# Kernel tuning notes

Hardware: AMD Instinct MI355X
Metric: run time of the kernel (lower is better)

## Reference

```python
import jax, jax.numpy as jnp
import numpy as np
from jax import lax

N_ROIS = 1024
ROI_H, ROI_W = 112, 224   # height divisible by 7; band = 16 rows
BANDS = 7
POOL_H, POOL_W = 8, 16    # adaptive max pool target
CONF_THRES = 0.25
PROV, ALPHA, AD = 38, 25, 35
FLAT = 16 * (POOL_H // 2) * (POOL_W // 2)  # 512 after conv+2x2 maxpool


def setup_inputs() -> dict:
    key = jax.random.key(0)
    ks = jax.random.split(key, 16)
    x = jax.random.normal(ks[0], (1, 3, 1024, 1024), dtype=jnp.float32)
    x1 = jax.random.randint(ks[1], (N_ROIS,), 0, 1024 - ROI_W)
    y1 = jax.random.randint(ks[2], (N_ROIS,), 0, 1024 - ROI_H)
    rois = jnp.stack([x1, y1, x1 + ROI_W, y1 + ROI_H], axis=-1).astype(jnp.int32)
    detection_targets = jax.random.randint(ks[3], (N_ROIS,), 0, PROV).astype(jnp.int32)
    classification_targets = jax.random.randint(ks[4], (N_ROIS, 8), 0, ALPHA).astype(jnp.int32)
    conv_w = jax.random.normal(ks[5], (16, 3, 3, 3), dtype=jnp.float32) * 0.1
    conv_b = jnp.zeros((16,), dtype=jnp.float32)
    w1 = jax.random.normal(ks[6], (8, FLAT, 128), dtype=jnp.float32) * 0.05
    b1 = jnp.zeros((8, 128), dtype=jnp.float32)
    w2_prov = jax.random.normal(ks[7], (128, PROV), dtype=jnp.float32) * 0.05
    b2_prov = jnp.zeros((PROV,), dtype=jnp.float32)
    w2_alpha = jax.random.normal(ks[8], (128, ALPHA), dtype=jnp.float32) * 0.05
    b2_alpha = jnp.zeros((ALPHA,), dtype=jnp.float32)
    w2_ad = jax.random.normal(ks[9], (6, 128, AD), dtype=jnp.float32) * 0.05
    b2_ad = jnp.zeros((6, AD), dtype=jnp.float32)
    return dict(x=x, rois=rois, detection_targets=detection_targets,
                classification_targets=classification_targets,
                conv_w=conv_w, conv_b=conv_b, w1=w1, b1=b1,
                w2_prov=w2_prov, b2_prov=b2_prov,
                w2_alpha=w2_alpha, b2_alpha=b2_alpha,
                w2_ad=w2_ad, b2_ad=b2_ad)


def _ce(logits, tgt):
    # per-row cross entropy; matches nn.CrossEntropyLoss on batch of 1 (mean==single)
    lp = jax.nn.log_softmax(logits, axis=-1)
    return -jnp.take_along_axis(lp, tgt[:, None], axis=1)[:, 0]


def _forward(x, rois, detection_targets, classification_targets,
             conv_w, conv_b, w1, b1, w2_prov, b2_prov,
             w2_alpha, b2_alpha, w2_ad, b2_ad):
    n = rois.shape[0]
    m = n * BANDS

    def extract(roi):
        return lax.dynamic_slice(x[0], (0, roi[1], roi[0]), (3, ROI_H, ROI_W))

    crops = jax.vmap(extract)(rois)                       # (N,3,112,224)
    band_h = ROI_H // BANDS                                # 16
    sub = crops.reshape(n, 3, BANDS, band_h, ROI_W)
    sub = sub.transpose(0, 2, 1, 3, 4).reshape(m, 3, band_h, ROI_W)  # (M,3,16,224)
    # adaptive max pool (16,224) -> (8,16): exact 2x14 windows
    pooled = sub.reshape(m, 3, POOL_H, band_h // POOL_H, POOL_W, ROI_W // POOL_W).max(axis=(3, 5))

    feat = lax.conv_general_dilated(pooled, conv_w, (1, 1), 'SAME',
                                    dimension_numbers=('NCHW', 'OIHW', 'NCHW'))
    feat = jax.nn.relu(feat + conv_b[None, :, None, None])  # (M,16,8,16)
    feat = feat.reshape(m, 16, POOL_H // 2, 2, POOL_W // 2, 2).max(axis=(3, 5))  # (M,16,4,8)
    flat = feat.reshape(m, FLAT)                             # (M,512)

    h = jax.nn.relu(jnp.einsum('md,kdh->kmh', flat, w1) + b1[:, None, :])  # (8,M,128)
    out_prov = h[0] @ w2_prov + b2_prov                      # (M,38)
    out_alpha = h[1] @ w2_alpha + b2_alpha                   # (M,25)
    out_ad = jnp.einsum('kmh,khc->kmc', h[2:], w2_ad) + b2_ad[:, None, :]  # (6,M,35)

    det_t = jnp.repeat(detection_targets, BANDS)             # (M,)
    det_loss = _ce(out_prov, det_t)
    mask = det_loss < CONF_THRES

    cls_t = jnp.repeat(classification_targets, BANDS, axis=0)  # (M,8)
    cls_loss = _ce(out_prov, cls_t[:, 0]) + _ce(out_alpha, cls_t[:, 1])
    cls_loss = cls_loss + jax.vmap(_ce)(out_ad, cls_t[:, 2:].T).sum(axis=0)
    total = jnp.sum(jnp.where(mask, cls_loss, 0.0))
    return out_prov, out_alpha, out_ad, mask, total


def reference(x, rois, detection_targets, classification_targets,
              conv_w, conv_b, w1, b1, w2_prov, b2_prov,
              w2_alpha, b2_alpha, w2_ad, b2_ad):
    return _forward(x, rois, detection_targets, classification_targets,
                    conv_w, conv_b, w1, b1, w2_prov, b2_prov,
                    w2_alpha, b2_alpha, w2_ad, b2_ad)
```

## Files before the change

### kernel.cpp

```cpp
#include <hip/hip_runtime.h>

#define NROIS 1024
#define BANDS 7
#define M_TOT (NROIS*BANDS)
#define ROI_W 224
#define BAND_H 16
#define FLATD 512
#define HD 1024
#define PROV 38
#define ALPHA 25
#define ADC 35
#define NAD 6

#define OFF_A     (M_TOT*PROV)
#define OFF_AD    (OFF_A + M_TOT*ALPHA)
#define OFF_MASK  (OFF_AD + NAD*M_TOT*ADC)
#define OFF_TOTAL (OFF_MASK + M_TOT)

typedef __attribute__((ext_vector_type(4))) float f32x4;
typedef __attribute__((ext_vector_type(2))) float f32x2;
typedef __attribute__((ext_vector_type(8))) short bf16x8;

static __device__ __forceinline__ unsigned short f2bf(float f){
    union { float f; unsigned int u; } v; v.f = f;
    unsigned int u = v.u;
    unsigned int r = (u + 0x7fffu + ((u >> 16) & 1u)) >> 16;
    return (unsigned short)r;
}

#define GL16(gp, lp) __builtin_amdgcn_global_load_lds( \
    (const __attribute__((address_space(1))) unsigned int*)(gp), \
    (__attribute__((address_space(3))) unsigned int*)(lp), 16, 0, 0)

#define P2ROW(c,row) (((size_t)((c)*1023 + (row)))*1022)

__global__ __launch_bounds__(256) void k_pre_cvt(
    const float* __restrict__ x, const float* __restrict__ w1,
    const float* __restrict__ w2p, const float* __restrict__ b2p,
    const float* __restrict__ w2a, const float* __restrict__ b2a,
    const float* __restrict__ w2ad, const float* __restrict__ b2ad,
    float* __restrict__ P, unsigned short* __restrict__ Bt,
    unsigned short* __restrict__ B2, float* __restrict__ bias2)
{
    __shared__ float v[1024];
    int blk = blockIdx.x;
    int t = threadIdx.x;
    if (blk < 3069){
        int c = blk / 1023, r = blk - c*1023;
        const float* row0 = x + ((size_t)c*1024 + r)*1024;
        const float* row1 = row0 + 1024;
        #pragma unroll
        for (int i=0;i<4;i++){
            int j = t + i*256;
            v[j] = fmaxf(row0[j], row1[j]);
        }
        __syncthreads();
        float* Pr = P + P2ROW(c, r);
        #pragma unroll
        for (int i=0;i<4;i++){
            int o = t + i*256;
            if (o < 1022){
                int s = o / 73, q = o - s*73;
                int j = 14*q + s;
                if (j < 1011){
                    float mv = v[j];
                    #pragma unroll
                    for (int d=1;d<14;d++) mv = fmaxf(mv, v[j+d]);
                    Pr[o] = mv;
                }
            }
        }
    } else {
        int i = (blk - 3069)*256 + t;
        if (i < 524288){
            int k = i >> 10, n = i & 1023;
            float val = w1[((size_t)(n>>7)*512 + k)*128 + (n&127)];
            Bt[(size_t)n*512 + k] = f2bf(val);
        } else {
            int j = i - 524288;
            int h = j / 6144;
            int rem = j - h*6144;
            int n = rem >> 7, k = rem & 127;
            float val = 0.f;
            if (h == 0){ if (n < 38) val = w2p[k*38 + n]; }
            else if (h == 1){ if (n < 25) val = w2a[k*25 + n]; }
            else { if (n < 35) val = w2ad[(size_t)(h-2)*128*35 + k*35 + n]; }
            B2[j] = f2bf(val);
            if (j < 8*48){
                int hh = j / 48, nn = j - hh*48;
                float bv = 0.f;
                if (hh == 0){ if (nn < 38) bv = b2p[nn]; }
                else if (hh == 1){ if (nn < 25) bv = b2a[nn]; }
                else { if (nn < 35) bv = b2ad[(hh-2)*35 + nn]; }
                bias2[j] = bv;
            }
        }
    }
}

__global__ __launch_bounds__(256) void k_extract(
    const float* __restrict__ P, const int* __restrict__ rois,
    const float* __restrict__ conv_w, const float* __restrict__ conv_b,
    unsigned short* __restrict__ flat)
{
    __shared__ float pl[3][10][20];
    __shared__ float cw[432];
    __shared__ float cb[16];

    int r = blockIdx.x;
    int t = threadIdx.x;
    int xx = rois[r*4+0];
    int y1 = rois[r*4+1];
    int sx = xx % 14, qx = xx / 14;
    int o2 = t >> 5, p = (t >> 3) & 3, q = t & 7;

    for (int i=t;i<432;i+=256) cw[i]=conv_w[i];
    if (t<16) cb[t]=conv_b[t];
    for (int i=t;i<3*10*20;i+=256) ((float*)pl)[i]=0.f;
    __syncthreads();

    float w[2][27];
    #pragma unroll
    for (int oi=0;oi<2;oi++){
        int o = o2 + oi*8;
        #pragma unroll
        for (int k=0;k<27;k++) w[oi][k] = cw[o*27 + k];
    }
    float bias0 = cb[o2], bias1 = cb[o2+8];

    for (int b=0; b<BANDS; b++){
        int yy = y1 + b*BAND_H;
        for (int idx=t; idx<384; idx+=256){
            int c = idx>>7; int rem = idx&127; int ph = rem>>4; int pw = rem&15;
            pl[c][ph+1][pw+1] = P[P2ROW(c, yy + 2*ph) + (size_t)sx*73 + qx + pw];
        }
        __syncthreads();

        float s0[4] = {bias0,bias0,bias0,bias0};
        float s1[4] = {bias1,bias1,bias1,bias1};
        #pragma unroll
        for (int c=0;c<3;c++){
            float pt[4][4];
            #pragma unroll
            for (int di=0; di<4; di++){
                f32x2 a = *(const f32x2*)&pl[c][2*p+di][2*q];
                f32x2 bb = *(const f32x2*)&pl[c][2*p+di][2*q+2];
                pt[di][0]=a.x; pt[di][1]=a.y; pt[di][2]=bb.x; pt[di][3]=bb.y;
            }
            #pragma unroll
            for (int kh=0;kh<3;kh++)
              #pragma unroll
              for (int kw=0;kw<3;kw++){
                float w0 = w[0][c*9+kh*3+kw];
                float w1v = w[1][c*9+kh*3+kw];
                #pragma unroll
                for (int pos=0;pos<4;pos++){
                    float pv = pt[kh + (pos>>1)][kw + (pos&1)];
                    s0[pos] += pv*w0;
                    s1[pos] += pv*w1v;
                }
              }
        }
        float mx0 = fmaxf(fmaxf(fmaxf(s0[0],s0[1]), fmaxf(s0[2],s0[3])), 0.f);
        float mx1 = fmaxf(fmaxf(fmaxf(s1[0],s1[1]), fmaxf(s1[2],s1[3])), 0.f);
        size_t base = ((size_t)r*BANDS + b)*512;
        flat[base + t]       = f2bf(mx0);
        flat[base + t + 256] = f2bf(mx1);
        __syncthreads();
    }
}

__global__ __launch_bounds__(256) void k_fc1_heads(
    const unsigned short* __restrict__ A, const unsigned short* __restrict__ Bt,
    const float* __restrict__ b1, const unsigned short* __restrict__ B2,
    const float* __restrict__ bias2, float* __restrict__ out,
    float* __restrict__ lse_ws)
{
    __shared__ short smem[16896];
    short* As = smem;
    short* Bs = smem + 8192;
    short* Hl = smem;

    int bm = blockIdx.x, h = blockIdx.y;
    int m0 = bm*128;
    int t = threadIdx.x;
    int wid = t >> 6, lane = t & 63;
    int wr = wid >> 1, wc = wid & 1;
    int l15 = lane & 15, l4 = lane >> 4;

    if (bm == 0 && h == 0 && t == 0) out[OFF_TOTAL] = 0.f;

    const unsigned short* gA = A  + ((size_t)(m0    + wid*16 + (lane>>2)))*FLATD + (lane&3)*8;
    const unsigned short* gB = Bt + ((size_t)(h*128 + wid*16 + (lane>>2)))*FLATD + (lane&3)*8;

    f32x4 acc[4][4];
    #pragma unroll
    for (int i=0;i<4;i++)
      #pragma unroll
      for (int j=0;j<4;j++) acc[i][j] = (f32x4){0.f,0.f,0.f,0.f};

    GL16(gA,            As + wid*512);
    GL16(gA + 64*FLATD, As + 2048 + wid*512);
    GL16(gB,            Bs + wid*512);
    GL16(gB + 64*FLATD, Bs + 2048 + wid*512);
    __syncthreads();

    #pragma unroll
    for (int ks=0; ks<16; ks++){
        int cur = ks & 1;
        if (ks < 15){
            int k1 = (ks+1)*32;
            int nb = (cur^1)*4096;
            GL16(gA + k1,            As + nb + wid*512);
            GL16(gA + 64*FLATD + k1, As + nb + 2048 + wid*512);
            GL16(gB + k1,            Bs + nb + wid*512);
            GL16(gB + 64*FLATD + k1, Bs + nb + 2048 + wid*512);
        }
        bf16x8 af[4], bfv[4];
        #pragma unroll
        for (int mf=0;mf<4;mf++) af[mf]  = *(const bf16x8*)&As[cur*4096 + (wr*64 + mf*16 + l15)*32 + l4*8];
        #pragma unroll
        for (int nf=0;nf<4;nf++) bfv[nf] = *(const bf16x8*)&Bs[cur*4096 + (wc*64 + nf*16 + l15)*32 + l4*8];
        #pragma unroll
        for (int mf=0;mf<4;mf++)
          #pragma unroll
          for (int nf=0;nf<4;nf++)
            acc[mf][nf] = __builtin_amdgcn_mfma_f32_16x16x32_bf16(af[mf], bfv[nf], acc[mf][nf], 0, 0, 0);
        __syncthreads();
    }

    #pragma unroll
    for (int nf=0;nf<4;nf++){
        int col = wc*64 + nf*16 + l15;
        float bias = b1[h*128 + col];
        #pragma unroll
        for (int mf=0;mf<4;mf++){
            #pragma unroll
            for (int reg=0;reg<4;reg++){
                int row = wr*64 + mf*16 + l4*4 + reg;
                Hl[row*132 + col] = (short)f2bf(fmaxf(acc[mf][nf][reg] + bias, 0.f));
            }
        }
    }
    __syncthreads();

    f32x4 acc2[2][3];
    #pragma unroll
    for (int i=0;i<2;i++)
      #pragma unroll
      for (int j=0;j<3;j++) acc2[i][j] = (f32x4){0.f,0.f,0.f,0.f};

    const unsigned short* Bh = B2 + (size_t)h*6144;
    #pragma unroll
    for (int ks=0; ks<4; ks++){
        bf16x8 ha[2], hb[3];
        #pragma unroll
        for (int m2=0;m2<2;m2++)
            ha[m2] = *(const bf16x8*)&Hl[(wid*32 + m2*16 + l15)*132 + ks*32 + l4*8];
        #pragma unroll
        for (int nf=0;nf<3;nf++)
            hb[nf] = *(const bf16x8*)(Bh + (nf*16 + l15)*128 + ks*32 + l4*8);
        #pragma unroll
        for (int m2=0;m2<2;m2++)
          #pragma unroll
          for (int nf=0;nf<3;nf++)
            acc2[m2][nf] = __builtin_amdgcn_mfma_f32_16x16x32_bf16(ha[m2], hb[nf], acc2[m2][nf], 0, 0, 0);
    }

    int Nh = (h==0) ? 38 : ((h==1) ? 25 : 35);
    #pragma unroll
    for (int nf=0;nf<3;nf++){
        int col = nf*16 + l15;
        float bv = bias2[h*48 + col];
        #pragma unroll
        for (int m2=0;m2<2;m2++){
            #pragma unroll
            for (int reg=0;reg<4;reg++){
                acc2[m2][nf][reg] += bv;
                if (col < Nh){
                    int m = m0 + wid*32 + m2*16 + l4*4 + reg;
                    size_t a;
                    if (h == 0)      a = (size_t)m*38 + col;
                    else if (h == 1) a = OFF_A + (size_t)m*25 + col;
                    else             a = OFF_AD + ((size_t)(h-2)*M_TOT + m)*35 + col;
                    out[a] = acc2[m2][nf][reg];
                }
            }
        }
    }

    #pragma unroll
    for (int m2=0;m2<2;m2++){
        #pragma unroll
        for (int reg=0;reg<4;reg++){
            float mx = -1e30f;
            #pragma unroll
            for (int nf=0;nf<3;nf++){
                int col = nf*16 + l15;
                if (col < Nh) mx = fmaxf(mx, acc2[m2][nf][reg]);
            }
            #pragma unroll
            for (int d=1; d<16; d<<=1) mx = fmaxf(mx, __shfl_xor(mx, d));
            float s = 0.f;
            #pragma unroll
            for (int nf=0;nf<3;nf++){
                int col = nf*16 + l15;
                if (col < Nh) s += __expf(acc2[m2][nf][reg] - mx);
            }
            #pragma unroll
            for (int d=1; d<16; d<<=1) s += __shfl_xor(s, d);
            if (l15 == 0){
                int m = m0 + wid*32 + m2*16 + l4*4 + reg;
                lse_ws[(size_t)m*8 + h] = mx + __logf(s);
            }
        }
    }
}

__global__ __launch_bounds__(256) void k_loss(
    const float* __restrict__ lse_ws, const int* __restrict__ det_t,
    const int* __restrict__ cls_t, float* __restrict__ out)
{
    int m = blockIdx.x*256 + threadIdx.x;
    if (m >= M_TOT) return;
    int r = m / 7;
    const float* L = lse_ws + (size_t)m*8;
    float det_loss = L[0] - out[(size_t)m*38 + det_t[r]];
    bool mk = det_loss < 0.25f;
    out[OFF_MASK + m] = mk ? 1.f : 0.f;
    if (mk){
        const int* ct = cls_t + r*8;
        float c = (L[0] - out[(size_t)m*38 + ct[0]]) + (L[1] - out[OFF_A + (size_t)m*25 + ct[1]]);
        #pragma unroll
        for (int j=0;j<6;j++)
            c += L[2+j] - out[OFF_AD + ((size_t)j*M_TOT + m)*35 + ct[2+j]];
        atomicAdd(out + OFF_TOTAL, c);
    }
}

extern "C" void kernel_launch(void* const* d_in, const int* in_sizes, int n_in,
                              void* d_out, int out_size, void* d_ws, size_t ws_size,
                              hipStream_t stream) {
    const float* x      = (const float*)d_in[0];
    const int*   rois   = (const int*)d_in[1];
    const int*   det    = (const int*)d_in[2];
    const int*   cls    = (const int*)d_in[3];
    const float* conv_w = (const float*)d_in[4];
    const float* conv_b = (const float*)d_in[5];
    const float* w1     = (const float*)d_in[6];
    const float* b1     = (const float*)d_in[7];
    const float* w2p    = (const float*)d_in[8];
    const float* b2p    = (const float*)d_in[9];
    const float* w2a    = (const float*)d_in[10];
    const float* b2a    = (const float*)d_in[11];
    const float* w2ad   = (const float*)d_in[12];
    const float* b2ad   = (const float*)d_in[13];
    float* out = (float*)d_out;

    char* w = (char*)d_ws;
    unsigned short* flatbf = (unsigned short*)w;
    unsigned short* BtW    = (unsigned short*)(w + 7340032);
    unsigned short* B2     = (unsigned short*)(w + 8388608);
    float*  bias2          = (float*)(w + 8486912);
    float*  lse            = (float*)(w + 8488448);
    float*  P              = (float*)(w + 8717824);

    k_pre_cvt<<<3069 + 2240, 256, 0, stream>>>(x, w1, w2p, b2p, w2a, b2a, w2ad, b2ad,
                                               P, BtW, B2, bias2);
    k_extract<<<NROIS, 256, 0, stream>>>(P, rois, conv_w, conv_b, flatbf);
    k_fc1_heads<<<dim3(56, 8), 256, 0, stream>>>(flatbf, BtW, b1, B2, bias2, out, lse);
    k_loss<<<28, 256, 0, stream>>>(lse, det, cls, out);
}
```

Before: 134.0 us.

## Triple-buffer fc1 GEMM with swizzled LDS, batch ROI band loads, share pooling windows

The fc1 GEMM now keeps three stages in flight instead of two, using explicit vmcnt waits and raw barriers, and XOR-swizzles its LDS layout to reduce bank conflicts. In k_extract all seven band tiles of a ROI are loaded into shared memory once up front, which removes the per-band barriers. The pooling step in k_pre_cvt computes two adjacent window outputs per thread and reuses their shared 13-element max. k_loss is launched with smaller blocks so more workgroups are spread across the device. These changes raise LDS use and rely on hand-set waitcnt values that have to match the number of issued loads.

Result: slower. 138.1 us (+3.0%).

```diff
diff --git a/kernel.cpp b/kernel.cpp
--- a/kernel.cpp
+++ b/kernel.cpp
@@ -57,16 +57,19 @@
         __syncthreads();
         float* Pr = P + P2ROW(c, r);
         #pragma unroll
-        for (int i=0;i<4;i++){
-            int o = t + i*256;
-            if (o < 1022){
-                int s = o / 73, q = o - s*73;
+        for (int ii=0; ii<2; ii++){
+            int i = t + ii*256;
+            if (i < 511){
+                int s2 = i / 73, q = i - s2*73;
+                int s = 2*s2;
                 int j = 14*q + s;
                 if (j < 1011){
-                    float mv = v[j];
+                    float core = v[j+1];
                     #pragma unroll
-                    for (int d=1;d<14;d++) mv = fmaxf(mv, v[j+d]);
-                    Pr[o] = mv;
+                    for (int d=2; d<14; d++) core = fmaxf(core, v[j+d]);
+                    Pr[s*73 + q] = fmaxf(core, v[j]);
+                    if (j+1 < 1011)
+                        Pr[(s+1)*73 + q] = fmaxf(core, v[j+14]);
                 }
             }
         }
@@ -103,7 +106,7 @@
     const float* __restrict__ conv_w, const float* __restrict__ conv_b,
     unsigned short* __restrict__ flat)
 {
-    __shared__ float pl[3][10][20];
+    __shared__ float pl[3][BANDS][10][20];
     __shared__ float cw[432];
     __shared__ float cb[16];
 
@@ -116,26 +119,27 @@
 
     for (int i=t;i<432;i+=256) cw[i]=conv_w[i];
     if (t<16) cb[t]=conv_b[t];
-    for (int i=t;i<3*10*20;i+=256) ((float*)pl)[i]=0.f;
+    for (int i=t;i<3*BANDS*10*20;i+=256) ((float*)pl)[i]=0.f;
     __syncthreads();
 
+    for (int idx=t; idx<3*BANDS*8*16; idx+=256){
+        int pw = idx & 15;
+        int rem = idx >> 4;
+        int ph = rem & 7;
+        int bb = (rem >> 3) % BANDS;
+        int c  = rem / (8*BANDS);
+        pl[c][bb][ph+1][pw+1] = P[P2ROW(c, y1 + bb*BAND_H + 2*ph) + (size_t)sx*73 + qx + pw];
+    }
+    __syncthreads();
+
     float w[2][27];
     #pragma unroll
-    for (int oi=0;oi<2;oi++){
-        int o = o2 + oi*8;
-        #pragma unroll
-        for (int k=0;k<27;k++) w[oi][k] = cw[o*27 + k];
-    }
+    for (int oi=0;oi<2;oi++)
+      #pragma unroll
+      for (int k=0;k<27;k++) w[oi][k] = cw[(o2 + oi*8)*27 + k];
     float bias0 = cb[o2], bias1 = cb[o2+8];
 
     for (int b=0; b<BANDS; b++){
-        int yy = y1 + b*BAND_H;
-        for (int idx=t; idx<384; idx+=256){
-            int c = idx>>7; int rem = idx&127; int ph = rem>>4; int pw = rem&15;
-            pl[c][ph+1][pw+1] = P[P2ROW(c, yy + 2*ph) + (size_t)sx*73 + qx + pw];
-        }
-        __syncthreads();
-
         float s0[4] = {bias0,bias0,bias0,bias0};
         float s1[4] = {bias1,bias1,bias1,bias1};
         #pragma unroll
@@ -143,9 +147,9 @@
             float pt[4][4];
             #pragma unroll
             for (int di=0; di<4; di++){
-                f32x2 a = *(const f32x2*)&pl[c][2*p+di][2*q];
-                f32x2 bb = *(const f32x2*)&pl[c][2*p+di][2*q+2];
-                pt[di][0]=a.x; pt[di][1]=a.y; pt[di][2]=bb.x; pt[di][3]=bb.y;
+                f32x2 a  = *(const f32x2*)&pl[c][b][2*p+di][2*q];
+                f32x2 bb2 = *(const f32x2*)&pl[c][b][2*p+di][2*q+2];
+                pt[di][0]=a.x; pt[di][1]=a.y; pt[di][2]=bb2.x; pt[di][3]=bb2.y;
             }
             #pragma unroll
             for (int kh=0;kh<3;kh++)
@@ -166,7 +170,6 @@
         size_t base = ((size_t)r*BANDS + b)*512;
         flat[base + t]       = f2bf(mx0);
         flat[base + t + 256] = f2bf(mx1);
-        __syncthreads();
     }
 }
 
@@ -176,9 +179,9 @@
     const float* __restrict__ bias2, float* __restrict__ out,
     float* __restrict__ lse_ws)
 {
-    __shared__ short smem[16896];
+    __shared__ short smem[24576];
     short* As = smem;
-    short* Bs = smem + 8192;
+    short* Bs = smem + 12288;
     short* Hl = smem;
 
     int bm = blockIdx.x, h = blockIdx.y;
@@ -190,8 +193,10 @@
 
     if (bm == 0 && h == 0 && t == 0) out[OFF_TOTAL] = 0.f;
 
-    const unsigned short* gA = A  + ((size_t)(m0    + wid*16 + (lane>>2)))*FLATD + (lane&3)*8;
-    const unsigned short* gB = Bt + ((size_t)(h*128 + wid*16 + (lane>>2)))*FLATD + (lane&3)*8;
+    int lrow = lane >> 2;
+    int lch  = (lane & 3) ^ (lrow & 3);
+    const unsigned short* gA = A  + ((size_t)(m0    + wid*16 + lrow))*FLATD + lch*8;
+    const unsigned short* gB = Bt + ((size_t)(h*128 + wid*16 + lrow))*FLATD + lch*8;
 
     f32x4 acc[4][4];
     #pragma unroll
@@ -199,35 +204,46 @@
       #pragma unroll
       for (int j=0;j<4;j++) acc[i][j] = (f32x4){0.f,0.f,0.f,0.f};
 
-    GL16(gA,            As + wid*512);
-    GL16(gA + 64*FLATD, As + 2048 + wid*512);
-    GL16(gB,            Bs + wid*512);
-    GL16(gB + 64*FLATD, Bs + 2048 + wid*512);
-    __syncthreads();
+#define STAGE(ks, buf) do { int _k0 = (ks)*32; \
+    GL16(gA + _k0,            As + (buf)*4096 + wid*512); \
+    GL16(gA + 64*FLATD + _k0, As + (buf)*4096 + 2048 + wid*512); \
+    GL16(gB + _k0,            Bs + (buf)*4096 + wid*512); \
+    GL16(gB + 64*FLATD + _k0, Bs + (buf)*4096 + 2048 + wid*512); } while(0)
+
+    STAGE(0, 0);
+    STAGE(1, 1);
 
     #pragma unroll
     for (int ks=0; ks<16; ks++){
-        int cur = ks & 1;
-        if (ks < 15){
-            int k1 = (ks+1)*32;
-            int nb = (cur^1)*4096;
-            GL16(gA + k1,            As + nb + wid*512);
-            GL16(gA + 64*FLATD + k1, As + nb + 2048 + wid*512);
-            GL16(gB + k1,            Bs + nb + wid*512);
-            GL16(gB + 64*FLATD + k1, Bs + nb + 2048 + wid*512);
-        }
+        if (ks < 14) STAGE(ks+2, (ks+2)%3);
+        if (ks < 14)       asm volatile("s_waitcnt vmcnt(8)" ::: "memory");
+        else if (ks == 14) asm volatile("s_waitcnt vmcnt(4)" ::: "memory");
+        else               asm volatile("s_waitcnt vmcnt(0)" ::: "memory");
+        __builtin_amdgcn_s_barrier();
+        __builtin_amdgcn_sched_barrier(0);
+        int cur = ks % 3;
         bf16x8 af[4], bfv[4];
         #pragma unroll
-        for (int mf=0;mf<4;mf++) af[mf]  = *(const bf16x8*)&As[cur*4096 + (wr*64 + mf*16 + l15)*32 + l4*8];
-        #pragma unroll
-        for (int nf=0;nf<4;nf++) bfv[nf] = *(const bf16x8*)&Bs[cur*4096 + (wc*64 + nf*16 + l15)*32 + l4*8];
+        for (int mf=0;mf<4;mf++){
+            int row = wr*64 + mf*16 + l15;
+            af[mf]  = *(const bf16x8*)&As[cur*4096 + row*32 + ((l4 ^ (l15&3))*8)];
+        }
+        #pragma unroll
+        for (int nf=0;nf<4;nf++){
+            int row = wc*64 + nf*16 + l15;
+            bfv[nf] = *(const bf16x8*)&Bs[cur*4096 + row*32 + ((l4 ^ (l15&3))*8)];
+        }
         #pragma unroll
         for (int mf=0;mf<4;mf++)
           #pragma unroll
           for (int nf=0;nf<4;nf++)
             acc[mf][nf] = __builtin_amdgcn_mfma_f32_16x16x32_bf16(af[mf], bfv[nf], acc[mf][nf], 0, 0, 0);
-        __syncthreads();
-    }
+        __builtin_amdgcn_sched_barrier(0);
+        __builtin_amdgcn_s_barrier();
+    }
+#undef STAGE
+
+    __syncthreads();
 
     #pragma unroll
     for (int nf=0;nf<4;nf++){
@@ -317,11 +333,11 @@
     }
 }
 
-__global__ __launch_bounds__(256) void k_loss(
+__global__ __launch_bounds__(64) void k_loss(
     const float* __restrict__ lse_ws, const int* __restrict__ det_t,
     const int* __restrict__ cls_t, float* __restrict__ out)
 {
-    int m = blockIdx.x*256 + threadIdx.x;
+    int m = blockIdx.x*64 + threadIdx.x;
     if (m >= M_TOT) return;
     int r = m / 7;
     const float* L = lse_ws + (size_t)m*8;
@@ -369,5 +385,5 @@
                                                P, BtW, B2, bias2);
     k_extract<<<NROIS, 256, 0, stream>>>(P, rois, conv_w, conv_b, flatbf);
     k_fc1_heads<<<dim3(56, 8), 256, 0, stream>>>(flatbf, BtW, b1, B2, bias2, out, lse);
-    k_loss<<<28, 256, 0, stream>>>(lse, det, cls, out);
-}
+    k_loss<<<112, 64, 0, stream>>>(lse, det, cls, out);
+}
```

## Tile w1 transpose through LDS, share pooling windows, preload all bands

Applied to the files above, without the earlier changes.

The w1 bf16 transpose now goes through a padded 64x64 LDS tile, so both global reads and writes are coalesced and far fewer blocks are launched. The horizontal 14-wide max pooling computes two adjacent outputs per thread that share 13 elements, roughly halving the LDS max work. k_extract loads all seven bands of pooled input into shared memory in one pass and drops the per-band barriers. k_loss uses smaller blocks to spread across more CUs. The costs are more shared memory per extract block and more complex index math.

Measured after the change: 137.0 us. 1.02x slower.

```diff
diff --git a/kernel.cpp b/kernel.cpp
--- a/kernel.cpp
+++ b/kernel.cpp
@@ -42,10 +42,11 @@
     float* __restrict__ P, unsigned short* __restrict__ Bt,
     unsigned short* __restrict__ B2, float* __restrict__ bias2)
 {
-    __shared__ float v[1024];
+    __shared__ float sm[64*65];
     int blk = blockIdx.x;
     int t = threadIdx.x;
     if (blk < 3069){
+        float* v = sm;
         int c = blk / 1023, r = blk - c*1023;
         const float* row0 = x + ((size_t)c*1024 + r)*1024;
         const float* row1 = row0 + 1024;
@@ -57,43 +58,59 @@
         __syncthreads();
         float* Pr = P + P2ROW(c, r);
         #pragma unroll
-        for (int i=0;i<4;i++){
-            int o = t + i*256;
-            if (o < 1022){
-                int s = o / 73, q = o - s*73;
+        for (int ii=0; ii<2; ii++){
+            int i = t + ii*256;
+            if (i < 511){
+                int s2 = i / 73, q = i - s2*73;
+                int s = 2*s2;
                 int j = 14*q + s;
                 if (j < 1011){
-                    float mv = v[j];
+                    float core = v[j+1];
                     #pragma unroll
-                    for (int d=1;d<14;d++) mv = fmaxf(mv, v[j+d]);
-                    Pr[o] = mv;
+                    for (int d=2; d<14; d++) core = fmaxf(core, v[j+d]);
+                    Pr[s*73 + q] = fmaxf(core, v[j]);
+                    if (j+1 < 1011)
+                        Pr[(s+1)*73 + q] = fmaxf(core, v[j+14]);
                 }
             }
         }
+    } else if (blk < 3197){
+        int tt = blk - 3069;
+        int h  = tt >> 4;
+        int rem = tt & 15;
+        int k0 = (rem >> 1) * 64;
+        int n0 = (rem & 1) * 64;
+        const float* W = w1 + (size_t)h*65536;
+        #pragma unroll
+        for (int e=0;e<16;e++){
+            int idx = e*256 + t;
+            int kk = idx >> 6, nn = idx & 63;
+            sm[kk*65 + nn] = W[(size_t)(k0+kk)*128 + n0 + nn];
+        }
+        __syncthreads();
+        #pragma unroll
+        for (int e=0;e<16;e++){
+            int idx = e*256 + t;
+            int nn = idx >> 6, kk = idx & 63;
+            Bt[(size_t)(h*128 + n0 + nn)*512 + k0 + kk] = f2bf(sm[kk*65 + nn]);
+        }
     } else {
-        int i = (blk - 3069)*256 + t;
-        if (i < 524288){
-            int k = i >> 10, n = i & 1023;
-            float val = w1[((size_t)(n>>7)*512 + k)*128 + (n&127)];
-            Bt[(size_t)n*512 + k] = f2bf(val);
-        } else {
-            int j = i - 524288;
-            int h = j / 6144;
-            int rem = j - h*6144;
-            int n = rem >> 7, k = rem & 127;
-            float val = 0.f;
-            if (h == 0){ if (n < 38) val = w2p[k*38 + n]; }
-            else if (h == 1){ if (n < 25) val = w2a[k*25 + n]; }
-            else { if (n < 35) val = w2ad[(size_t)(h-2)*128*35 + k*35 + n]; }
-            B2[j] = f2bf(val);
-            if (j < 8*48){
-                int hh = j / 48, nn = j - hh*48;
-                float bv = 0.f;
-                if (hh == 0){ if (nn < 38) bv = b2p[nn]; }
-                else if (hh == 1){ if (nn < 25) bv = b2a[nn]; }
-                else { if (nn < 35) bv = b2ad[(hh-2)*35 + nn]; }
-                bias2[j] = bv;
-            }
+        int j = (blk - 3197)*256 + t;
+        int h = j / 6144;
+        int rem = j - h*6144;
+        int n = rem >> 7, k = rem & 127;
+        float val = 0.f;
+        if (h == 0){ if (n < 38) val = w2p[k*38 + n]; }
+        else if (h == 1){ if (n < 25) val = w2a[k*25 + n]; }
+        else { if (n < 35) val = w2ad[(size_t)(h-2)*128*35 + k*35 + n]; }
+        B2[j] = f2bf(val);
+        if (j < 8*48){
+            int hh = j / 48, nn = j - hh*48;
+            float bv = 0.f;
+            if (hh == 0){ if (nn < 38) bv = b2p[nn]; }
+            else if (hh == 1){ if (nn < 25) bv = b2a[nn]; }
+            else { if (nn < 35) bv = b2ad[(hh-2)*35 + nn]; }
+            bias2[j] = bv;
         }
     }
 }
@@ -103,7 +120,7 @@
     const float* __restrict__ conv_w, const float* __restrict__ conv_b,
     unsigned short* __restrict__ flat)
 {
-    __shared__ float pl[3][10][20];
+    __shared__ float pl[3][BANDS][10][20];
     __shared__ float cw[432];
     __shared__ float cb[16];
 
@@ -116,26 +133,27 @@
 
     for (int i=t;i<432;i+=256) cw[i]=conv_w[i];
     if (t<16) cb[t]=conv_b[t];
-    for (int i=t;i<3*10*20;i+=256) ((float*)pl)[i]=0.f;
+    for (int i=t;i<3*BANDS*10*20;i+=256) ((float*)pl)[i]=0.f;
     __syncthreads();
 
+    for (int idx=t; idx<3*BANDS*8*16; idx+=256){
+        int pw = idx & 15;
+        int rem = idx >> 4;
+        int ph = rem & 7;
+        int bb = (rem >> 3) % BANDS;
+        int c  = rem / (8*BANDS);
+        pl[c][bb][ph+1][pw+1] = P[P2ROW(c, y1 + bb*BAND_H + 2*ph) + (size_t)sx*73 + qx + pw];
+    }
+    __syncthreads();
+
     float w[2][27];
     #pragma unroll
-    for (int oi=0;oi<2;oi++){
-        int o = o2 + oi*8;
-        #pragma unroll
-        for (int k=0;k<27;k++) w[oi][k] = cw[o*27 + k];
-    }
+    for (int oi=0;oi<2;oi++)
+      #pragma unroll
+      for (int k=0;k<27;k++) w[oi][k] = cw[(o2 + oi*8)*27 + k];
     float bias0 = cb[o2], bias1 = cb[o2+8];
 
     for (int b=0; b<BANDS; b++){
-        int yy = y1 + b*BAND_H;
-        for (int idx=t; idx<384; idx+=256){
-            int c = idx>>7; int rem = idx&127; int ph = rem>>4; int pw = rem&15;
-            pl[c][ph+1][pw+1] = P[P2ROW(c, yy + 2*ph) + (size_t)sx*73 + qx + pw];
-        }
-        __syncthreads();
-
         float s0[4] = {bias0,bias0,bias0,bias0};
         float s1[4] = {bias1,bias1,bias1,bias1};
         #pragma unroll
@@ -143,9 +161,9 @@
             float pt[4][4];
             #pragma unroll
             for (int di=0; di<4; di++){
-                f32x2 a = *(const f32x2*)&pl[c][2*p+di][2*q];
-                f32x2 bb = *(const f32x2*)&pl[c][2*p+di][2*q+2];
-                pt[di][0]=a.x; pt[di][1]=a.y; pt[di][2]=bb.x; pt[di][3]=bb.y;
+                f32x2 a   = *(const f32x2*)&pl[c][b][2*p+di][2*q];
+                f32x2 bb2 = *(const f32x2*)&pl[c][b][2*p+di][2*q+2];
+                pt[di][0]=a.x; pt[di][1]=a.y; pt[di][2]=bb2.x; pt[di][3]=bb2.y;
             }
             #pragma unroll
             for (int kh=0;kh<3;kh++)
@@ -166,7 +184,6 @@
         size_t base = ((size_t)r*BANDS + b)*512;
         flat[base + t]       = f2bf(mx0);
         flat[base + t + 256] = f2bf(mx1);
-        __syncthreads();
     }
 }
 
@@ -317,11 +334,11 @@
     }
 }
 
-__global__ __launch_bounds__(256) void k_loss(
+__global__ __launch_bounds__(64) void k_loss(
     const float* __restrict__ lse_ws, const int* __restrict__ det_t,
     const int* __restrict__ cls_t, float* __restrict__ out)
 {
-    int m = blockIdx.x*256 + threadIdx.x;
+    int m = blockIdx.x*64 + threadIdx.x;
     if (m >= M_TOT) return;
     int r = m / 7;
     const float* L = lse_ws + (size_t)m*8;
@@ -365,9 +382,9 @@
     float*  lse            = (float*)(w + 8488448);
     float*  P              = (float*)(w + 8717824);
 
-    k_pre_cvt<<<3069 + 2240, 256, 0, stream>>>(x, w1, w2p, b2p, w2a, b2a, w2ad, b2ad,
-                                               P, BtW, B2, bias2);
+    k_pre_cvt<<<3069 + 128 + 192, 256, 0, stream>>>(x, w1, w2p, b2p, w2a, b2a, w2ad, b2ad,
+                                                    P, BtW, B2, bias2);
     k_extract<<<NROIS, 256, 0, stream>>>(P, rois, conv_w, conv_b, flatbf);
     k_fc1_heads<<<dim3(56, 8), 256, 0, stream>>>(flatbf, BtW, b1, B2, bias2, out, lse);
-    k_loss<<<28, 256, 0, stream>>>(lse, det, cls, out);
-}
+    k_loss<<<112, 64, 0, stream>>>(lse, det, cls, out);
+}
```
